# Optimization experiments

Measured on AMD Instinct MI355X. Metric: run time of the kernel, lower is better.

Reference implementation:

```python
import jax, jax.numpy as jnp
import numpy as np

B, S, D = 4, 2048, 1024
NEG = -1e9

def setup_inputs() -> dict:
    key = jax.random.key(0)
    ks = jax.random.split(key, 12)
    sc = 1.0 / np.sqrt(D)
    inp = {
        'query': jax.random.normal(ks[0], (B, S, D), jnp.float32),
        'key':   jax.random.normal(ks[1], (B, S, D), jnp.float32),
        'value': jax.random.normal(ks[2], (B, S, D), jnp.float32),
        'Wq': jax.random.normal(ks[3], (D, D), jnp.float32) * sc,
        'bq': jnp.zeros((D,), jnp.float32),
        'Wk': jax.random.normal(ks[4], (D, D), jnp.float32) * sc,
        'bk': jnp.zeros((D,), jnp.float32),
        'Wv': jax.random.normal(ks[5], (D, D), jnp.float32) * sc,
        'bv': jnp.zeros((D,), jnp.float32),
        'Wo': jax.random.normal(ks[6], (D, D), jnp.float32) * sc,
        'bo': jnp.zeros((D,), jnp.float32),
    }
    return inp

def reference(query, key, value, Wq, bq, Wk, bk, Wv, bv, Wo, bo):
    d_model = query.shape[-1]
    q = query @ Wq + bq            # [B,S,D]
    k = key   @ Wk + bk
    v = value @ Wv + bv
    # scores scaled by sqrt(d_model) (single head, full d_model)
    scores = jnp.einsum('bqd,bkd->bqk', q, k) / jnp.sqrt(jnp.float32(d_model))
    s = scores.shape[-1]
    causal = jnp.tril(jnp.ones((s, s), bool))  # True = keep
    scores = jnp.where(causal, scores, NEG)
    # log-softmax then exp for numerical stability (use_log_probs=True)
    attn = jnp.exp(jax.nn.log_softmax(scores, axis=-1))
    out = jnp.einsum('bqk,bkd->bqd', attn, v)
    return out @ Wo + bo
```

## Files before the change

### kernel.cpp

```cpp
#include <hip/hip_runtime.h>


typedef __attribute__((ext_vector_type(8))) short bf16x8_t;
typedef __attribute__((ext_vector_type(4))) float f32x4_t;

static __device__ __forceinline__ unsigned short f2b(float f) {
  union { float f; unsigned u; } c; c.f = f;
  unsigned u = c.u;
  u += 0x7fffu + ((u >> 16) & 1u);
  return (unsigned short)(u >> 16);
}

static __device__ __forceinline__ void gload16(const void* g, const void* l) {
  __builtin_amdgcn_global_load_lds(
      (const __attribute__((address_space(1))) void*)g,
      (__attribute__((address_space(3))) void*)(void*)(unsigned short*)l,
      16, 0, 0);
}

template<bool A_IS_F32, bool HAS_BIAS, bool OUT_BF16>
static __device__ __forceinline__
void gemm_body(const void* __restrict__ Ap, const unsigned short* __restrict__ Bt,
               const float* __restrict__ bias, void* __restrict__ Cp,
               int kEnd, int lda, int ldb, int ldc, float scale, int bx, int by)
{
  __shared__ unsigned short As[128 * 64];
  __shared__ unsigned short Bs[128 * 64];

  const int tid  = threadIdx.x;
  const int lane = tid & 63;
  const int wid  = tid >> 6;
  const int wr   = wid >> 1, wc = wid & 1;
  const int l15  = lane & 15, l4 = lane >> 4;

  const float*          Af = (const float*)Ap;
  const unsigned short* Ab = (const unsigned short*)Ap;

  const int srow_l = lane >> 3;
  const int schk   = lane & 7;
  const int frow = tid >> 3;
  const int fchk = tid & 7;

  f32x4_t acc[4][4];
#pragma unroll
  for (int m = 0; m < 4; ++m)
#pragma unroll
    for (int n = 0; n < 4; ++n) acc[m][n] = (f32x4_t){0.f, 0.f, 0.f, 0.f};

  for (int k0 = 0; k0 < kEnd; k0 += 64) {
    if (A_IS_F32) {
#pragma unroll
      for (int i = 0; i < 4; ++i) {
        const int row = i * 32 + frow;
        const size_t gr = (size_t)(by * 128 + row);
        const float* src = Af + gr * lda + k0 + fchk * 8;
        const float4 x0 = *(const float4*)src;
        const float4 x1 = *(const float4*)(src + 4);
        union { unsigned short s[8]; uint4 v; } pk;
        pk.s[0] = f2b(x0.x); pk.s[1] = f2b(x0.y); pk.s[2] = f2b(x0.z); pk.s[3] = f2b(x0.w);
        pk.s[4] = f2b(x1.x); pk.s[5] = f2b(x1.y); pk.s[6] = f2b(x1.z); pk.s[7] = f2b(x1.w);
        const int c = fchk ^ (row & 7);
        *(uint4*)&As[row * 64 + c * 8] = pk.v;
      }
    } else {
#pragma unroll
      for (int i = 0; i < 4; ++i) {
        const int row = i * 32 + wid * 8 + srow_l;
        const size_t gr = (size_t)(by * 128 + row);
        const int g = schk ^ (row & 7);
        gload16(Ab + gr * lda + k0 + g * 8, &As[(i * 32 + wid * 8) * 64]);
      }
    }
#pragma unroll
    for (int i = 0; i < 4; ++i) {
      const int row = i * 32 + wid * 8 + srow_l;
      const size_t gn = (size_t)(bx * 128 + row);
      const int g = schk ^ (row & 7);
      gload16(Bt + gn * ldb + k0 + g * 8, &Bs[(i * 32 + wid * 8) * 64]);
    }
    __syncthreads();

#pragma unroll
    for (int kk = 0; kk < 2; ++kk) {
      bf16x8_t a[4], b[4];
#pragma unroll
      for (int m = 0; m < 4; ++m) {
        const int row = wr * 64 + m * 16 + l15;
        const int c = (kk * 4 + l4) ^ (row & 7);
        a[m] = *(const bf16x8_t*)&As[row * 64 + c * 8];
      }
#pragma unroll
      for (int n = 0; n < 4; ++n) {
        const int row = wc * 64 + n * 16 + l15;
        const int c = (kk * 4 + l4) ^ (row & 7);
        b[n] = *(const bf16x8_t*)&Bs[row * 64 + c * 8];
      }
#pragma unroll
      for (int m = 0; m < 4; ++m)
#pragma unroll
        for (int n = 0; n < 4; ++n)
          acc[m][n] = __builtin_amdgcn_mfma_f32_16x16x32_bf16(a[m], b[n], acc[m][n], 0, 0, 0);
    }
    __syncthreads();
  }

  float*          Cf = (float*)Cp;
  unsigned short* Cb = (unsigned short*)Cp;
#pragma unroll
  for (int m = 0; m < 4; ++m)
#pragma unroll
    for (int n = 0; n < 4; ++n) {
      const int col = bx * 128 + wc * 64 + n * 16 + l15;
      const float bv = HAS_BIAS ? bias[col] : 0.f;
#pragma unroll
      for (int j = 0; j < 4; ++j) {
        const int row = by * 128 + wr * 64 + m * 16 + l4 * 4 + j;
        const float val = acc[m][n][j] * scale + bv;
        if (OUT_BF16) Cb[(size_t)row * ldc + col] = f2b(val);
        else          Cf[(size_t)row * ldc + col] = val;
      }
    }
}

__global__ __launch_bounds__(256)
void gemm_qkv(const float* __restrict__ q, const float* __restrict__ k,
              const float* __restrict__ v,
              const unsigned short* __restrict__ Wq,
              const unsigned short* __restrict__ Wk,
              const unsigned short* __restrict__ Wv,
              const float* __restrict__ bq, const float* __restrict__ bk,
              const float* __restrict__ bv,
              unsigned short* __restrict__ oq, unsigned short* __restrict__ ok,
              unsigned short* __restrict__ ov)
{
  const int z = blockIdx.z;
  const float* A = z == 0 ? q : (z == 1 ? k : v);
  const unsigned short* B = z == 0 ? Wq : (z == 1 ? Wk : Wv);
  const float* bias = z == 0 ? bq : (z == 1 ? bk : bv);
  unsigned short* C = z == 0 ? oq : (z == 1 ? ok : ov);
  gemm_body<true, true, true>(A, B, bias, C, 1024, 1024, 1024, 1024, 1.f,
                              blockIdx.x, blockIdx.y);
}

__global__ __launch_bounds__(256)
void gemm_scores(const unsigned short* __restrict__ Q,
                 const unsigned short* __restrict__ Kb, float* __restrict__ S)
{
  const int bz = blockIdx.z;
  const int t = blockIdx.x;
  int by = (int)((sqrtf(8.f * t + 1.f) - 1.f) * 0.5f);
  while ((by + 1) * (by + 2) / 2 <= t) ++by;
  while (by * (by + 1) / 2 > t) --by;
  const int bx = t - by * (by + 1) / 2;
  gemm_body<false, false, false>(Q + (size_t)bz * 2048 * 1024,
                                 Kb + (size_t)bz * 2048 * 1024, nullptr,
                                 S + (size_t)bz * 2048 * 2048,
                                 1024, 1024, 1024, 2048, 0.03125f, bx, by);
}

__global__ __launch_bounds__(256)
void gemm_pv(const unsigned short* __restrict__ P,
             const unsigned short* __restrict__ Vt, unsigned short* __restrict__ C)
{
  const int bz = blockIdx.z, bx = blockIdx.x, by = blockIdx.y;
  const int kEnd = (by + 1) * 128;
  gemm_body<false, false, true>(P + (size_t)bz * 2048 * 4096,
                                Vt + (size_t)bz * 1024 * 2048, nullptr,
                                C + (size_t)bz * 2048 * 1024,
                                kEnd, 4096, 2048, 1024, 1.f, bx, by);
}

__global__ __launch_bounds__(256)
void gemm_out(const unsigned short* __restrict__ ctx,
              const unsigned short* __restrict__ Wo,
              const float* __restrict__ bo, float* __restrict__ out)
{
  gemm_body<false, true, false>(ctx, Wo, bo, out, 1024, 1024, 1024, 1024, 1.f,
                                blockIdx.x, blockIdx.y);
}

__global__ __launch_bounds__(256)
void transpose4_w(const float* __restrict__ w0, const float* __restrict__ w1,
                  const float* __restrict__ w2, const float* __restrict__ w3,
                  unsigned short* __restrict__ o0, unsigned short* __restrict__ o1,
                  unsigned short* __restrict__ o2, unsigned short* __restrict__ o3)
{
  __shared__ unsigned short t[32][34];
  const int z = blockIdx.z;
  const float* in = z == 0 ? w0 : (z == 1 ? w1 : (z == 2 ? w2 : w3));
  unsigned short* out = z == 0 ? o0 : (z == 1 ? o1 : (z == 2 ? o2 : o3));
  const int bx = blockIdx.x, by = blockIdx.y;
  const int x = threadIdx.x, y = threadIdx.y;
#pragma unroll
  for (int yy = y; yy < 32; yy += 8)
    t[yy][x] = f2b(in[(size_t)(by * 32 + yy) * 1024 + bx * 32 + x]);
  __syncthreads();
#pragma unroll
  for (int yy = y; yy < 32; yy += 8)
    out[(size_t)(bx * 32 + yy) * 1024 + by * 32 + x] = t[x][yy];
}

__global__ __launch_bounds__(256)
void transpose_v(const unsigned short* __restrict__ in, unsigned short* __restrict__ out)
{
  __shared__ unsigned short t[32][34];
  const int bx = blockIdx.x;
  const int by = blockIdx.y;
  const int bz = blockIdx.z;
  const int x = threadIdx.x, y = threadIdx.y;
  const unsigned short* inb = in + (size_t)bz * 2048 * 1024;
  unsigned short* ob = out + (size_t)bz * 1024 * 2048;
#pragma unroll
  for (int yy = y; yy < 32; yy += 8)
    t[yy][x] = inb[(size_t)(by * 32 + yy) * 1024 + bx * 32 + x];
  __syncthreads();
#pragma unroll
  for (int yy = y; yy < 32; yy += 8)
    ob[(size_t)(bx * 32 + yy) * 2048 + by * 32 + x] = t[x][yy];
}

__global__ __launch_bounds__(256)
void softmax_rows(const float* __restrict__ S, unsigned short* __restrict__ P)
{
  const int row = blockIdx.x;
  const int q = row & 2047;
  const float* srow = S + (size_t)row * 2048;
  unsigned short* prow = P + (size_t)row * 4096;
  const int nvalid = q + 1;
  const int kend = ((q >> 7) + 1) << 7;
  const int tid = threadIdx.x;
  const int wid = tid >> 6, lane = tid & 63;
  const int base = tid * 8;

  const float4 x0 = *(const float4*)(srow + base);
  const float4 x1 = *(const float4*)(srow + base + 4);
  float v[8] = {x0.x, x0.y, x0.z, x0.w, x1.x, x1.y, x1.z, x1.w};

  float m = -1e30f;
#pragma unroll
  for (int i = 0; i < 8; ++i) {
    if (base + i >= nvalid) v[i] = -1e30f;
    m = fmaxf(m, v[i]);
  }
#pragma unroll
  for (int off = 32; off > 0; off >>= 1) m = fmaxf(m, __shfl_xor(m, off));
  __shared__ float redm[4];
  __shared__ float reds[4];
  if (lane == 0) redm[wid] = m;
  __syncthreads();
  m = fmaxf(fmaxf(redm[0], redm[1]), fmaxf(redm[2], redm[3]));

  float s = 0.f;
  float e[8];
#pragma unroll
  for (int i = 0; i < 8; ++i) {
    e[i] = (base + i < nvalid) ? __expf(v[i] - m) : 0.f;
    s += e[i];
  }
#pragma unroll
  for (int off = 32; off > 0; off >>= 1) s += __shfl_xor(s, off);
  if (lane == 0) reds[wid] = s;
  __syncthreads();
  s = reds[0] + reds[1] + reds[2] + reds[3];
  const float inv = 1.f / s;

  if (base < kend) {
    union { unsigned u[4]; uint4 v4; } pk;
#pragma unroll
    for (int i = 0; i < 4; ++i) {
      const unsigned lo = f2b(e[2 * i] * inv);
      const unsigned hi = f2b(e[2 * i + 1] * inv);
      pk.u[i] = lo | (hi << 16);
    }
    *(uint4*)(prow + base) = pk.v4;
  }
}

extern "C" void kernel_launch(void* const* d_in, const int* in_sizes, int n_in,
                              void* d_out, int out_size, void* d_ws, size_t ws_size,
                              hipStream_t stream)
{
  const float* query = (const float*)d_in[0];
  const float* key   = (const float*)d_in[1];
  const float* value = (const float*)d_in[2];
  const float* Wq    = (const float*)d_in[3];
  const float* bq    = (const float*)d_in[4];
  const float* Wk    = (const float*)d_in[5];
  const float* bk    = (const float*)d_in[6];
  const float* Wv    = (const float*)d_in[7];
  const float* bv    = (const float*)d_in[8];
  const float* Wo    = (const float*)d_in[9];
  const float* bo    = (const float*)d_in[10];
  float* out = (float*)d_out;

  char* ws = (char*)d_ws;
  const size_t MB = 1024 * 1024;
  unsigned short* Wqt  = (unsigned short*)(ws + 0 * MB);
  unsigned short* Wkt  = (unsigned short*)(ws + 2 * MB);
  unsigned short* Wvt  = (unsigned short*)(ws + 4 * MB);
  unsigned short* Wot  = (unsigned short*)(ws + 6 * MB);
  unsigned short* qbuf = (unsigned short*)(ws + 8 * MB);
  unsigned short* kbuf = (unsigned short*)(ws + 24 * MB);
  unsigned short* vbuf = (unsigned short*)(ws + 40 * MB);
  unsigned short* vT   = (unsigned short*)(ws + 56 * MB);
  float*          Sraw = (float*)(ws + 72 * MB);
  unsigned short* ctx  = (unsigned short*)(ws + 136 * MB);

  transpose4_w<<<dim3(32, 32, 4), dim3(32, 8), 0, stream>>>(
      Wq, Wk, Wv, Wo, Wqt, Wkt, Wvt, Wot);

  gemm_qkv<<<dim3(8, 64, 3), 256, 0, stream>>>(
      query, key, value, Wqt, Wkt, Wvt, bq, bk, bv, qbuf, kbuf, vbuf);

  transpose_v<<<dim3(32, 64, 4), dim3(32, 8), 0, stream>>>(vbuf, vT);

  gemm_scores<<<dim3(136, 1, 4), 256, 0, stream>>>(qbuf, kbuf, Sraw);

  softmax_rows<<<8192, 256, 0, stream>>>(Sraw, (unsigned short*)Sraw);

  gemm_pv<<<dim3(8, 16, 4), 256, 0, stream>>>((unsigned short*)Sraw, vT, ctx);

  gemm_out<<<dim3(8, 64, 1), 256, 0, stream>>>(ctx, Wot, bo, out);
}
```

Baseline: 397.6 us.

## Pre-cast QKV inputs to bf16 and remap GEMM blocks across XCDs

Adds a separate kernel that casts query/key/value to bf16, so the QKV GEMM can stage its A tiles with async global-to-LDS loads instead of per-tile fp32 loads and conversion. It also flattens all GEMM grids to 1D and remaps block indices so that consecutive tiles sharing an A row-panel land on the same XCD, aiming for better L2 reuse. The cast costs an extra kernel launch and an extra round trip of the inputs through memory. The bf16 input buffers reuse workspace that Sraw later overwrites.

```diff
diff --git a/kernel.cpp b/kernel.cpp
--- a/kernel.cpp
+++ b/kernel.cpp
@@ -18,9 +18,30 @@
       16, 0, 0);
 }
 
-template<bool A_IS_F32, bool HAS_BIAS, bool OUT_BF16>
+__global__ __launch_bounds__(256)
+void cast3_bf16(const float* __restrict__ q, const float* __restrict__ k,
+                const float* __restrict__ v,
+                unsigned short* __restrict__ oq, unsigned short* __restrict__ ok,
+                unsigned short* __restrict__ ov)
+{
+  const int z = blockIdx.z;
+  const float* in = z == 0 ? q : (z == 1 ? k : v);
+  unsigned short* out = z == 0 ? oq : (z == 1 ? ok : ov);
+  const size_t base = ((size_t)blockIdx.x * 256 + threadIdx.x) * 8;
+  const float4 x0 = *(const float4*)(in + base);
+  const float4 x1 = *(const float4*)(in + base + 4);
+  union { unsigned u[4]; uint4 v4; } pk;
+  pk.u[0] = f2b(x0.x) | ((unsigned)f2b(x0.y) << 16);
+  pk.u[1] = f2b(x0.z) | ((unsigned)f2b(x0.w) << 16);
+  pk.u[2] = f2b(x1.x) | ((unsigned)f2b(x1.y) << 16);
+  pk.u[3] = f2b(x1.z) | ((unsigned)f2b(x1.w) << 16);
+  *(uint4*)(out + base) = pk.v4;
+}
+
+template<bool HAS_BIAS, bool OUT_BF16>
 static __device__ __forceinline__
-void gemm_body(const void* __restrict__ Ap, const unsigned short* __restrict__ Bt,
+void gemm_body(const unsigned short* __restrict__ Ab,
+               const unsigned short* __restrict__ Bt,
                const float* __restrict__ bias, void* __restrict__ Cp,
                int kEnd, int lda, int ldb, int ldc, float scale, int bx, int by)
 {
@@ -33,13 +54,8 @@
   const int wr   = wid >> 1, wc = wid & 1;
   const int l15  = lane & 15, l4 = lane >> 4;
 
-  const float*          Af = (const float*)Ap;
-  const unsigned short* Ab = (const unsigned short*)Ap;
-
   const int srow_l = lane >> 3;
   const int schk   = lane & 7;
-  const int frow = tid >> 3;
-  const int fchk = tid & 7;
 
   f32x4_t acc[4][4];
 #pragma unroll
@@ -48,28 +64,12 @@
     for (int n = 0; n < 4; ++n) acc[m][n] = (f32x4_t){0.f, 0.f, 0.f, 0.f};
 
   for (int k0 = 0; k0 < kEnd; k0 += 64) {
-    if (A_IS_F32) {
-#pragma unroll
-      for (int i = 0; i < 4; ++i) {
-        const int row = i * 32 + frow;
-        const size_t gr = (size_t)(by * 128 + row);
-        const float* src = Af + gr * lda + k0 + fchk * 8;
-        const float4 x0 = *(const float4*)src;
-        const float4 x1 = *(const float4*)(src + 4);
-        union { unsigned short s[8]; uint4 v; } pk;
-        pk.s[0] = f2b(x0.x); pk.s[1] = f2b(x0.y); pk.s[2] = f2b(x0.z); pk.s[3] = f2b(x0.w);
-        pk.s[4] = f2b(x1.x); pk.s[5] = f2b(x1.y); pk.s[6] = f2b(x1.z); pk.s[7] = f2b(x1.w);
-        const int c = fchk ^ (row & 7);
-        *(uint4*)&As[row * 64 + c * 8] = pk.v;
-      }
-    } else {
-#pragma unroll
-      for (int i = 0; i < 4; ++i) {
-        const int row = i * 32 + wid * 8 + srow_l;
-        const size_t gr = (size_t)(by * 128 + row);
-        const int g = schk ^ (row & 7);
-        gload16(Ab + gr * lda + k0 + g * 8, &As[(i * 32 + wid * 8) * 64]);
-      }
+#pragma unroll
+    for (int i = 0; i < 4; ++i) {
+      const int row = i * 32 + wid * 8 + srow_l;
+      const size_t gr = (size_t)(by * 128 + row);
+      const int g = schk ^ (row & 7);
+      gload16(Ab + gr * lda + k0 + g * 8, &As[(i * 32 + wid * 8) * 64]);
     }
 #pragma unroll
     for (int i = 0; i < 4; ++i) {
@@ -123,8 +123,9 @@
 }
 
 __global__ __launch_bounds__(256)
-void gemm_qkv(const float* __restrict__ q, const float* __restrict__ k,
-              const float* __restrict__ v,
+void gemm_qkv(const unsigned short* __restrict__ qi,
+              const unsigned short* __restrict__ ki,
+              const unsigned short* __restrict__ vi,
               const unsigned short* __restrict__ Wq,
               const unsigned short* __restrict__ Wk,
               const unsigned short* __restrict__ Wv,
@@ -133,41 +134,52 @@
               unsigned short* __restrict__ oq, unsigned short* __restrict__ ok,
               unsigned short* __restrict__ ov)
 {
-  const int z = blockIdx.z;
-  const float* A = z == 0 ? q : (z == 1 ? k : v);
+  const int d = blockIdx.x;
+  const int xcd = d & 7, j = d >> 3;
+  const int G = xcd * 24 + (j >> 3);
+  const int z = G >> 6;
+  const int by = G & 63;
+  const int bx = j & 7;
+  const unsigned short* A = z == 0 ? qi : (z == 1 ? ki : vi);
   const unsigned short* B = z == 0 ? Wq : (z == 1 ? Wk : Wv);
   const float* bias = z == 0 ? bq : (z == 1 ? bk : bv);
   unsigned short* C = z == 0 ? oq : (z == 1 ? ok : ov);
-  gemm_body<true, true, true>(A, B, bias, C, 1024, 1024, 1024, 1024, 1.f,
-                              blockIdx.x, blockIdx.y);
+  gemm_body<true, true>(A, B, bias, C, 1024, 1024, 1024, 1024, 1.f, bx, by);
 }
 
 __global__ __launch_bounds__(256)
 void gemm_scores(const unsigned short* __restrict__ Q,
                  const unsigned short* __restrict__ Kb, float* __restrict__ S)
 {
-  const int bz = blockIdx.z;
-  const int t = blockIdx.x;
-  int by = (int)((sqrtf(8.f * t + 1.f) - 1.f) * 0.5f);
-  while ((by + 1) * (by + 2) / 2 <= t) ++by;
-  while (by * (by + 1) / 2 > t) --by;
-  const int bx = t - by * (by + 1) / 2;
-  gemm_body<false, false, false>(Q + (size_t)bz * 2048 * 1024,
-                                 Kb + (size_t)bz * 2048 * 1024, nullptr,
-                                 S + (size_t)bz * 2048 * 2048,
-                                 1024, 1024, 1024, 2048, 0.03125f, bx, by);
+  const int d = blockIdx.x;
+  const int t = (d & 7) * 68 + (d >> 3);
+  const int bz = t / 136;
+  const int tri = t - bz * 136;
+  int by = (int)((sqrtf(8.f * tri + 1.f) - 1.f) * 0.5f);
+  while ((by + 1) * (by + 2) / 2 <= tri) ++by;
+  while (by * (by + 1) / 2 > tri) --by;
+  const int bx = tri - by * (by + 1) / 2;
+  gemm_body<false, false>(Q + (size_t)bz * 2048 * 1024,
+                          Kb + (size_t)bz * 2048 * 1024, nullptr,
+                          S + (size_t)bz * 2048 * 2048,
+                          1024, 1024, 1024, 2048, 0.03125f, bx, by);
 }
 
 __global__ __launch_bounds__(256)
 void gemm_pv(const unsigned short* __restrict__ P,
              const unsigned short* __restrict__ Vt, unsigned short* __restrict__ C)
 {
-  const int bz = blockIdx.z, bx = blockIdx.x, by = blockIdx.y;
+  const int d = blockIdx.x;
+  const int xcd = d & 7, j = d >> 3;
+  const int G = xcd * 8 + (j >> 3);
+  const int bz = G >> 4;
+  const int by = G & 15;
+  const int bx = j & 7;
   const int kEnd = (by + 1) * 128;
-  gemm_body<false, false, true>(P + (size_t)bz * 2048 * 4096,
-                                Vt + (size_t)bz * 1024 * 2048, nullptr,
-                                C + (size_t)bz * 2048 * 1024,
-                                kEnd, 4096, 2048, 1024, 1.f, bx, by);
+  gemm_body<false, true>(P + (size_t)bz * 2048 * 4096,
+                         Vt + (size_t)bz * 1024 * 2048, nullptr,
+                         C + (size_t)bz * 2048 * 1024,
+                         kEnd, 4096, 2048, 1024, 1.f, bx, by);
 }
 
 __global__ __launch_bounds__(256)
@@ -175,8 +187,11 @@
               const unsigned short* __restrict__ Wo,
               const float* __restrict__ bo, float* __restrict__ out)
 {
-  gemm_body<false, true, false>(ctx, Wo, bo, out, 1024, 1024, 1024, 1024, 1.f,
-                                blockIdx.x, blockIdx.y);
+  const int d = blockIdx.x;
+  const int xcd = d & 7, j = d >> 3;
+  const int by = xcd * 8 + (j >> 3);
+  const int bx = j & 7;
+  gemm_body<true, false>(ctx, Wo, bo, out, 1024, 1024, 1024, 1024, 1.f, bx, by);
 }
 
 __global__ __launch_bounds__(256)
@@ -304,21 +319,26 @@
   unsigned short* vbuf = (unsigned short*)(ws + 40 * MB);
   unsigned short* vT   = (unsigned short*)(ws + 56 * MB);
   float*          Sraw = (float*)(ws + 72 * MB);
+  unsigned short* qin  = (unsigned short*)(ws + 72 * MB);
+  unsigned short* kin  = (unsigned short*)(ws + 88 * MB);
+  unsigned short* vin  = (unsigned short*)(ws + 104 * MB);
   unsigned short* ctx  = (unsigned short*)(ws + 136 * MB);
+
+  cast3_bf16<<<dim3(4096, 1, 3), 256, 0, stream>>>(query, key, value, qin, kin, vin);
 
   transpose4_w<<<dim3(32, 32, 4), dim3(32, 8), 0, stream>>>(
       Wq, Wk, Wv, Wo, Wqt, Wkt, Wvt, Wot);
 
-  gemm_qkv<<<dim3(8, 64, 3), 256, 0, stream>>>(
-      query, key, value, Wqt, Wkt, Wvt, bq, bk, bv, qbuf, kbuf, vbuf);
+  gemm_qkv<<<1536, 256, 0, stream>>>(
+      qin, kin, vin, Wqt, Wkt, Wvt, bq, bk, bv, qbuf, kbuf, vbuf);
 
   transpose_v<<<dim3(32, 64, 4), dim3(32, 8), 0, stream>>>(vbuf, vT);
 
-  gemm_scores<<<dim3(136, 1, 4), 256, 0, stream>>>(qbuf, kbuf, Sraw);
+  gemm_scores<<<544, 256, 0, stream>>>(qbuf, kbuf, Sraw);
 
   softmax_rows<<<8192, 256, 0, stream>>>(Sraw, (unsigned short*)Sraw);
 
-  gemm_pv<<<dim3(8, 16, 4), 256, 0, stream>>>((unsigned short*)Sraw, vT, ctx);
-
-  gemm_out<<<dim3(8, 64, 1), 256, 0, stream>>>(ctx, Wot, bo, out);
-}
+  gemm_pv<<<512, 256, 0, stream>>>((unsigned short*)Sraw, vT, ctx);
+
+  gemm_out<<<512, 256, 0, stream>>>(ctx, Wot, bo, out);
+}
```

After: 347.2 us. -12.7%, faster.
